# Kernel tuning notes

Hardware: AMD Instinct MI355X
Metric: run time of the kernel (lower is better)

## Reference

```python
import jax, jax.numpy as jnp
import numpy as np

D, H, W = 128, 96, 96  # voxel grid
EPS = 1e-5

_OFFS = np.array([[dz, dy, dx] for dz in (-1, 0, 1) for dy in (-1, 0, 1) for dx in (-1, 0, 1)], dtype=np.int64)


def _flat(c):
    return (c[:, 0] * H + c[:, 1]) * W + c[:, 2]


def _dilate(coords):
    # union of coords + all 27 offsets, clipped to grid bounds (stride-1, pad-1 SparseConv3d output sites)
    p = coords[None, :, :] + _OFFS[:, None, :]          # [27, N, 3]
    p = p.reshape(-1, 3)
    ok = np.all((p >= 0) & (p < np.array([D, H, W])), axis=1)
    keys = np.unique(_flat(p[ok]))
    out = np.stack([keys // (H * W), (keys // W) % H, keys % W], axis=1)
    return out


def _rulebook(in_coords, out_coords):
    # nb[k, m] = row index into in_coords of (out_coords[m] + off_k), or -1
    lut = -np.ones(D * H * W, dtype=np.int32)
    lut[_flat(in_coords)] = np.arange(len(in_coords), dtype=np.int32)
    nb = np.full((27, len(out_coords)), -1, dtype=np.int32)
    for k, o in enumerate(_OFFS):
        p = out_coords + o
        ok = np.all((p >= 0) & (p < np.array([D, H, W])), axis=1)
        nb[k, ok] = lut[_flat(p[ok])]
    return nb


def setup_inputs() -> dict:
    key = jax.random.key(0)
    ks = jax.random.split(key, 20)
    # active sites: full plane z=64 over 96x96 footprint (surface-like sparse scene)
    yy, xx = np.meshgrid(np.arange(H), np.arange(W), indexing='ij')
    coords0 = np.stack([np.full(H * W, 64), yy.ravel(), xx.ravel()], axis=1).astype(np.int64)
    coords1 = _dilate(coords0)   # 27648 sites
    coords2 = _dilate(coords1)   # 46080 sites
    nb1 = jnp.asarray(_rulebook(coords0, coords1))
    nbs = jnp.asarray(_rulebook(coords1, coords1))
    nb2 = jnp.asarray(_rulebook(coords1, coords2))

    s = 0.05
    inp = {
        'x': jax.random.normal(ks[0], (coords0.shape[0], 256), jnp.float32),
        'w_s1': jax.random.normal(ks[1], (27, 256, 128), jnp.float32) * s,
        'g_s1': jax.random.uniform(ks[2], (128,), jnp.float32, 0.5, 1.5),
        'b_s1': jax.random.normal(ks[3], (128,), jnp.float32) * 0.1,
        'w11': jax.random.normal(ks[4], (27, 128, 128), jnp.float32) * s,
        'g11': jax.random.uniform(ks[5], (128,), jnp.float32, 0.5, 1.5),
        'b11': jax.random.normal(ks[6], (128,), jnp.float32) * 0.1,
        'w12': jax.random.normal(ks[7], (27, 128, 128), jnp.float32) * s,
        'g12': jax.random.uniform(ks[8], (128,), jnp.float32, 0.5, 1.5),
        'b12': jax.random.normal(ks[9], (128,), jnp.float32) * 0.1,
        'w21': jax.random.normal(ks[10], (27, 128, 128), jnp.float32) * s,
        'g21': jax.random.uniform(ks[11], (128,), jnp.float32, 0.5, 1.5),
        'b21': jax.random.normal(ks[12], (128,), jnp.float32) * 0.1,
        'w22': jax.random.normal(ks[13], (27, 128, 128), jnp.float32) * s,
        'g22': jax.random.uniform(ks[14], (128,), jnp.float32, 0.5, 1.5),
        'b22': jax.random.normal(ks[15], (128,), jnp.float32) * 0.1,
        'w_s2': jax.random.normal(ks[16], (27, 128, 32), jnp.float32) * s,
        'g_s2': jax.random.uniform(ks[17], (32,), jnp.float32, 0.5, 1.5),
        'b_s2': jax.random.normal(ks[18], (32,), jnp.float32) * 0.1,
        'nb1': nb1, 'nbs': nbs, 'nb2': nb2,
    }
    return inp


def _sparse_conv(x, nb, w):
    # gather -> GEMM -> accumulate per kernel offset (rulebook semantics of spconv)
    mask = nb >= 0                      # [27, M]
    idx = jnp.where(mask, nb, 0)
    out = jnp.zeros((nb.shape[1], w.shape[2]), x.dtype)
    for k in range(nb.shape[0]):        # fixed 27-offset loop
        g = jnp.where(mask[k][:, None], x[idx[k]], 0.0)  # [M, Cin]
        out = out + g @ w[k]
    return out


def _bn(f, g, b):
    # BatchNorm1d in training mode over active voxel rows (biased variance)
    mu = jnp.mean(f, axis=0)
    var = jnp.mean(jnp.square(f - mu), axis=0)
    return (f - mu) * jax.lax.rsqrt(var + EPS) * g + b


def _block(f, nbs, w1, g1, b1, w2, g2, b2):
    idn = f
    h = jax.nn.relu(_bn(_sparse_conv(f, nbs, w1), g1, b1))
    h = _bn(_sparse_conv(h, nbs, w2), g2, b2)
    return jax.nn.relu(h + idn)


def reference(x, w_s1, g_s1, b_s1, w11, g11, b11, w12, g12, b12,
              w21, g21, b21, w22, g22, b22, w_s2, g_s2, b_s2,
              nb1, nbs, nb2):
    f = jax.nn.relu(_bn(_sparse_conv(x, nb1, w_s1), g_s1, b_s1))          # spconv1
    f = _block(f, nbs, w11, g11, b11, w12, g12, b12)                      # block1 (submanifold)
    f = _block(f, nbs, w21, g21, b21, w22, g22, b22)                      # block2 (submanifold)
    out = jax.nn.relu(_bn(_sparse_conv(f, nb2, w_s2), g_s2, b_s2))        # spconv2
    return out  # features of the final SparseConvTensor, [46080, 32]
```

## Files before the change

### kernel.cpp

```cpp
#include <hip/hip_runtime.h>
#include <stdint.h>

typedef _Float16 f16;
typedef _Float16 f16x8 __attribute__((ext_vector_type(8)));
typedef _Float16 f16x4 __attribute__((ext_vector_type(4)));
typedef float f32x4 __attribute__((ext_vector_type(4)));

#define GAS __attribute__((address_space(1)))
#define LAS __attribute__((address_space(3)))

__device__ __forceinline__ void gl_lds16(const void* g, void* l) {
    __builtin_amdgcn_global_load_lds((const GAS uint32_t*)g, (LAS uint32_t*)l, 16, 0, 0);
}

__global__ __launch_bounds__(256) void prep(
    const float* __restrict__ x, f16* __restrict__ xh, long nx4,
    const float* __restrict__ ws1, f16* __restrict__ w1,
    const float* __restrict__ w11, f16* __restrict__ wa1,
    const float* __restrict__ w12, f16* __restrict__ wa2,
    const float* __restrict__ w21, f16* __restrict__ wb1,
    const float* __restrict__ w22, f16* __restrict__ wb2,
    const float* __restrict__ ws2, f16* __restrict__ w2,
    float* __restrict__ zbuf, long nz, int nbzc) {
    if ((int)blockIdx.x < nbzc) {
        long t = (long)blockIdx.x * 256 + threadIdx.x;
        if (t < nz) { zbuf[t] = 0.f; return; }
        t -= nz;
        if (t < nx4) {
            float4 v = ((const float4*)x)[t];
            f16x4 o = {(f16)v.x, (f16)v.y, (f16)v.z, (f16)v.w};
            *(f16x4*)(xh + t * 4) = o;
        }
        return;
    }
    int tau = blockIdx.x - nbzc;
    const float* src; f16* dst; int Cin, Cout;
    if (tau < 864)        { src = ws1; dst = w1;  Cin = 256; Cout = 128; }
    else if (tau < 1296)  { tau -= 864;  src = w11; dst = wa1; Cin = 128; Cout = 128; }
    else if (tau < 1728)  { tau -= 1296; src = w12; dst = wa2; Cin = 128; Cout = 128; }
    else if (tau < 2160)  { tau -= 1728; src = w21; dst = wb1; Cin = 128; Cout = 128; }
    else if (tau < 2592)  { tau -= 2160; src = w22; dst = wb2; Cin = 128; Cout = 128; }
    else                  { tau -= 2592; src = ws2; dst = w2;  Cin = 128; Cout = 32; }
    const int nci = Cin >> 5, nco = Cout >> 5;
    const int k  = tau / (nci * nco);
    const int rm = tau - k * nci * nco;
    const int ci0 = (rm / nco) << 5;
    const int co0 = (rm % nco) << 5;
    __shared__ float tile[32][33];
    const int r = threadIdx.x >> 5, c = threadIdx.x & 31;
#pragma unroll
    for (int i2 = 0; i2 < 4; i2++)
        tile[r + 8 * i2][c] =
            src[((long)(k * Cin + ci0 + r + 8 * i2)) * Cout + co0 + c];
    __syncthreads();
#pragma unroll
    for (int i2 = 0; i2 < 4; i2++)
        dst[((long)(k * Cout + co0 + r + 8 * i2)) * Cin + ci0 + c] =
            (f16)tile[c][r + 8 * i2];
}

template <int LAYER>
__global__ __launch_bounds__(512, 2) void conv_dense(
    const f16* __restrict__ fin, const f16* __restrict__ wt,
    const f16* __restrict__ zrow, float* __restrict__ out,
    float* __restrict__ stats) {
    constexpr int COUT = (LAYER == 2) ? 32 : 128;
    constexpr int INRB = (LAYER == 0) ? 512 : 256;
    constexpr int WRB  = (LAYER == 0) ? 512 : 256;
    constexpr int RT   = (COUT == 128) ? 4 : 2;
    constexpr int CT   = (COUT == 128) ? 4 : 2;
    constexpr int NBCH = COUT / 4;
    extern __shared__ char smem[];
    char* ldsA0 = smem;
    char* ldsA1 = smem + 46080;
    char* ldsB0 = smem + 92160;
    char* ldsB1 = smem + 92160 + COUT * 256;

    const int b = blockIdx.x;
    const int p = b / 72;
    const int t0 = b % 72;
    const int y0 = (t0 / 6) * 8;
    const int x0 = (t0 % 6) * 16;
    const int tid = threadIdx.x;
    const int lane = tid & 63;
    const int wave = tid >> 6;
    const int kh = wave & 1;
    const int pairId = wave >> 1;
    const int q = lane >> 4;
    const int r16 = lane & 15;
    const int wr = ((COUT == 128) ? (pairId >> 1) : pairId) * (RT * 16);
    const int wc = ((COUT == 128) ? (pairId & 1) : 0) * (CT * 16);

    int S = 0;
    int js[3], dzs[3], hs[3];
    if (LAYER == 0) {
        js[0] = 0; dzs[0] = 1 - p; hs[0] = 0;
        js[1] = 0; dzs[1] = 1 - p; hs[1] = 1;
        S = 2;
    } else {
        for (int dz = -1; dz <= 1; dz++) {
            int j = (LAYER == 1) ? p + dz : p + dz - 1;
            if (0 <= j && j < 3) { js[S] = j; dzs[S] = dz; hs[S] = 0; S++; }
        }
    }

    auto stageA = [&](int s, char* buf) {
        const int j = js[s], h = hs[s];
        const long pbase = (long)j * 9216;
        for (int ch = wave; ch < 45; ch += 8) {
            int site = ch * 4 + q;
            int sy = site / 18;
            int sx = site - sy * 18;
            int y = y0 - 1 + sy;
            int x = x0 - 1 + sx;
            int cc = r16 ^ (site & 7);
            bool ok = ((unsigned)y < 96u) & ((unsigned)x < 96u);
            const char* src = ok
                ? (const char*)fin + (pbase + y * 96 + x) * INRB + h * 256 + cc * 16
                : (const char*)zrow + cc * 16;
            gl_lds16(src, buf + ch * 1024);
        }
    };
    auto stageB = [&](int k, int h, char* buf) {
        for (int ch = wave; ch < NBCH; ch += 8) {
            int col = ch * 4 + q;
            int cc = r16 ^ (col & 7);
            const char* src = (const char*)wt + (long)(k * COUT + col) * WRB +
                              h * 256 + cc * 16;
            gl_lds16(src, buf + ch * 1024);
        }
    };

    f32x4 acc[RT][CT];
#pragma unroll
    for (int tr = 0; tr < RT; tr++)
#pragma unroll
        for (int c = 0; c < CT; c++) acc[tr][c] = f32x4{0.f, 0.f, 0.f, 0.f};

    stageA(0, ldsA0);
    stageB((dzs[0] + 1) * 9, hs[0], ldsB0);

    int tap = 0;
    for (int s = 0; s < S; s++) {
        const char* bufA = (s & 1) ? ldsA1 : ldsA0;
#pragma unroll
        for (int i = 0; i < 9; i++, tap++) {
            __syncthreads();
            if (i == 0 && s + 1 < S) stageA(s + 1, ((s + 1) & 1) ? ldsA1 : ldsA0);
            if (tap + 1 < S * 9) {
                int sn = (i == 8) ? s + 1 : s;
                int in2 = (i == 8) ? 0 : i + 1;
                stageB((dzs[sn] + 1) * 9 + in2, hs[sn], ((tap + 1) & 1) ? ldsB1 : ldsB0);
            }
            const char* bufB = (tap & 1) ? ldsB1 : ldsB0;
            const int dy = i / 3 - 1, dx = i % 3 - 1;
#pragma unroll
            for (int kk2 = 0; kk2 < 2; kk2++) {
                const int kk = kh * 2 + kk2;
                f16x8 Af[RT], Bf[CT];
#pragma unroll
                for (int tr = 0; tr < RT; tr++) {
                    int site = (wr / 16 + tr + 1 + dy) * 18 + 1 + dx + r16;
                    Af[tr] = *(const f16x8*)(bufA + site * 256 +
                                             (((kk * 4 + q) ^ (site & 7)) << 4));
                }
#pragma unroll
                for (int c = 0; c < CT; c++) {
                    int col = wc + c * 16 + r16;
                    Bf[c] = *(const f16x8*)(bufB + col * 256 +
                                            (((kk * 4 + q) ^ (col & 7)) << 4));
                }
#pragma unroll
                for (int tr = 0; tr < RT; tr++)
#pragma unroll
                    for (int c = 0; c < CT; c++)
                        acc[tr][c] = __builtin_amdgcn_mfma_f32_16x16x32_f16(
                            Af[tr], Bf[c], acc[tr][c], 0, 0, 0);
            }
        }
    }

    char* xch = smem + 92160;
    constexpr int XR = RT * CT * 1024;
    __syncthreads();
    if (kh == 1) {
#pragma unroll
        for (int tr = 0; tr < RT; tr++)
#pragma unroll
            for (int c = 0; c < CT; c++)
                *(f32x4*)(xch + pairId * XR + (tr * CT + c) * 1024 + lane * 16) =
                    acc[tr][c];
    }
    __syncthreads();
    if (kh == 1) return;
#pragma unroll
    for (int tr = 0; tr < RT; tr++)
#pragma unroll
        for (int c = 0; c < CT; c++)
            acc[tr][c] += *(const f32x4*)(xch + pairId * XR + (tr * CT + c) * 1024 +
                                          lane * 16);

    const long mbase = (long)p * 9216 + (long)y0 * 96 + x0;
#pragma unroll
    for (int c = 0; c < CT; c++) {
        const int col = wc + c * 16 + r16;
        float sum = 0.f, ssq = 0.f;
#pragma unroll
        for (int tr = 0; tr < RT; tr++) {
            const int ly = wr / 16 + tr;
#pragma unroll
            for (int r = 0; r < 4; r++) {
                const int lx = q * 4 + r;
                float v = acc[tr][c][r];
                out[(mbase + ly * 96 + lx) * COUT + col] = v;
                sum += v;
                ssq = fmaf(v, v, ssq);
            }
        }
        sum += __shfl_xor(sum, 16);
        sum += __shfl_xor(sum, 32);
        ssq += __shfl_xor(ssq, 16);
        ssq += __shfl_xor(ssq, 32);
        if (q == 0) {
            atomicAdd(&stats[col], sum);
            atomicAdd(&stats[COUT + col], ssq);
        }
    }
}

__global__ __launch_bounds__(256) void bn_apply4(
    const float4* __restrict__ f, const float* __restrict__ sums,
    const float* __restrict__ g, const float* __restrict__ bta,
    const f16x4* __restrict__ idn, f16* __restrict__ outh,
    float4* __restrict__ outf, long n4, int C, float invM) {
    long i = (long)blockIdx.x * 256 + threadIdx.x;
    if (i >= n4) return;
    int col0 = (int)((i * 4) & (C - 1));
    float4 v = f[i];
    float r[4] = {v.x, v.y, v.z, v.w};
    f16x4 id = {};
    if (idn) id = idn[i];
    f16x4 ho;
#pragma unroll
    for (int j = 0; j < 4; j++) {
        int c = col0 + j;
        float mu = sums[c] * invM;
        float var = sums[C + c] * invM - mu * mu;
        var = fmaxf(var, 0.f);
        float sc = g[c] * rsqrtf(var + 1e-5f);
        float x = (r[j] - mu) * sc + bta[c];
        if (idn) x += (float)id[j];
        x = fmaxf(x, 0.f);
        r[j] = x;
        ho[j] = (f16)x;
    }
    if (outf) outf[i] = make_float4(r[0], r[1], r[2], r[3]);
    else *(f16x4*)(outh + i * 4) = ho;
}

extern "C" void kernel_launch(void* const* d_in, const int* in_sizes, int n_in,
                              void* d_out, int out_size, void* d_ws, size_t ws_size,
                              hipStream_t stream) {
    (void)n_in; (void)out_size; (void)ws_size;
    const float* x    = (const float*)d_in[0];
    const float* w_s1 = (const float*)d_in[1];
    const float* g_s1 = (const float*)d_in[2];
    const float* b_s1 = (const float*)d_in[3];
    const float* w11  = (const float*)d_in[4];
    const float* g11  = (const float*)d_in[5];
    const float* b11  = (const float*)d_in[6];
    const float* w12  = (const float*)d_in[7];
    const float* g12  = (const float*)d_in[8];
    const float* b12  = (const float*)d_in[9];
    const float* w21  = (const float*)d_in[10];
    const float* g21  = (const float*)d_in[11];
    const float* b21  = (const float*)d_in[12];
    const float* w22  = (const float*)d_in[13];
    const float* g22  = (const float*)d_in[14];
    const float* b22  = (const float*)d_in[15];
    const float* w_s2 = (const float*)d_in[16];
    const float* g_s2 = (const float*)d_in[17];
    const float* b_s2 = (const float*)d_in[18];

    const int N0 = in_sizes[0] / 256;
    const int M1 = in_sizes[19] / 27;
    const int M2 = in_sizes[21] / 27;

    char* base = (char*)d_ws;
    size_t off = 0;
    auto alloc = [&](size_t bytes) -> char* {
        off = (off + 255) & ~(size_t)255;
        char* p = base + off;
        off += bytes;
        return p;
    };
    f16* xh  = (f16*)alloc((size_t)N0 * 256 * 2);
    f16* w1  = (f16*)alloc(27UL * 128 * 256 * 2);
    f16* wa1 = (f16*)alloc(27UL * 128 * 128 * 2);
    f16* wa2 = (f16*)alloc(27UL * 128 * 128 * 2);
    f16* wb1 = (f16*)alloc(27UL * 128 * 128 * 2);
    f16* wb2 = (f16*)alloc(27UL * 128 * 128 * 2);
    f16* w2  = (f16*)alloc(27UL * 32 * 128 * 2);
    f16* fA  = (f16*)alloc((size_t)M1 * 128 * 2);
    f16* fB  = (f16*)alloc((size_t)M1 * 128 * 2);
    float* cbuf  = (float*)alloc((size_t)M1 * 128 * 4);
    float* stats = (float*)alloc(1344UL * 4);
    f16*   zrow  = (f16*)alloc(512);

    const int lds01 = 92160 + 2 * 128 * 256;
    const int lds2  = 92160 + 2 * 32 * 256;
    (void)hipFuncSetAttribute((const void*)conv_dense<0>,
                              hipFuncAttributeMaxDynamicSharedMemorySize, lds01);
    (void)hipFuncSetAttribute((const void*)conv_dense<1>,
                              hipFuncAttributeMaxDynamicSharedMemorySize, lds01);
    (void)hipFuncSetAttribute((const void*)conv_dense<2>,
                              hipFuncAttributeMaxDynamicSharedMemorySize, lds2);

    const long nz  = 1472;
    const long nx4 = (long)N0 * 256 / 4;
    const int nbzc = (int)((nz + nx4 + 255) / 256);
    prep<<<nbzc + 2700, 256, 0, stream>>>(
        x, xh, nx4, w_s1, w1, w11, wa1, w12, wa2, w21, wb1, w22, wb2,
        w_s2, w2, stats, nz, nbzc);

    const float inv1 = 1.f / (float)M1, inv2 = 1.f / (float)M2;
    const int g1 = 3 * 72;
    const int g2 = 5 * 72;
    const long n4a = (long)M1 * 128 / 4;
    const long n4b = (long)M2 * 32 / 4;
    const int ga = (int)((n4a + 255) / 256);
    const int gb = (int)((n4b + 255) / 256);

    conv_dense<0><<<g1, 512, lds01, stream>>>(xh, w1, zrow, cbuf, stats);
    bn_apply4<<<ga, 256, 0, stream>>>((float4*)cbuf, stats, g_s1, b_s1,
                                      nullptr, fA, nullptr, n4a, 128, inv1);
    conv_dense<1><<<g1, 512, lds01, stream>>>(fA, wa1, zrow, cbuf, stats + 256);
    bn_apply4<<<ga, 256, 0, stream>>>((float4*)cbuf, stats + 256, g11, b11,
                                      nullptr, fB, nullptr, n4a, 128, inv1);
    conv_dense<1><<<g1, 512, lds01, stream>>>(fB, wa2, zrow, cbuf, stats + 512);
    bn_apply4<<<ga, 256, 0, stream>>>((float4*)cbuf, stats + 512, g12, b12,
                                      (const f16x4*)fA, fA, nullptr, n4a, 128, inv1);
    conv_dense<1><<<g1, 512, lds01, stream>>>(fA, wb1, zrow, cbuf, stats + 768);
    bn_apply4<<<ga, 256, 0, stream>>>((float4*)cbuf, stats + 768, g21, b21,
                                      nullptr, fB, nullptr, n4a, 128, inv1);
    conv_dense<1><<<g1, 512, lds01, stream>>>(fB, wb2, zrow, cbuf, stats + 1024);
    bn_apply4<<<ga, 256, 0, stream>>>((float4*)cbuf, stats + 1024, g22, b22,
                                      (const f16x4*)fA, fA, nullptr, n4a, 128, inv1);
    conv_dense<2><<<g2, 512, lds2, stream>>>(fA, w2, zrow, cbuf, stats + 1280);
    bn_apply4<<<gb, 256, 0, stream>>>((float4*)cbuf, stats + 1280, g_s2, b_s2,
                                      nullptr, nullptr, (float4*)d_out, n4b, 32, inv2);
}
```

Measured before the change: 378.1 us.

## Fold BatchNorm+ReLU of previous layer into conv input staging, store raw outputs fp16

Conv outputs are now stored as fp16 instead of fp32, halving the raw-output write and read traffic. For the second conv of each block and for the final spconv, the previous layer's BN scale/shift, ReLU and optional residual add are applied while staging input tiles into LDS. This removes three bn_apply passes. The cost is that these layers use register loads plus LDS stores instead of async global-to-LDS copies, and every halo site is normalised again by each tile that reads it. Storing raw pre-BN values in fp16 also adds some rounding error.

```diff
diff --git a/kernel.cpp b/kernel.cpp
--- a/kernel.cpp
+++ b/kernel.cpp
@@ -59,11 +59,14 @@
             (f16)tile[c][r + 8 * i2];
 }
 
-template <int LAYER>
+template <int LAYER, bool FOLD, bool RESID>
 __global__ __launch_bounds__(512, 2) void conv_dense(
     const f16* __restrict__ fin, const f16* __restrict__ wt,
-    const f16* __restrict__ zrow, float* __restrict__ out,
-    float* __restrict__ stats) {
+    const f16* __restrict__ zrow, f16* __restrict__ out,
+    float* __restrict__ stats,
+    const float* __restrict__ pstats, const float* __restrict__ pg,
+    const float* __restrict__ pb, const f16* __restrict__ resid,
+    float pinv) {
     constexpr int COUT = (LAYER == 2) ? 32 : 128;
     constexpr int INRB = (LAYER == 0) ? 512 : 256;
     constexpr int WRB  = (LAYER == 0) ? 512 : 256;
@@ -104,6 +107,19 @@
         }
     }
 
+    float psc[8], pbt[8];
+    if (FOLD) {
+#pragma unroll
+        for (int e = 0; e < 8; e++) {
+            int c = r16 * 8 + e;
+            float mu = pstats[c] * pinv;
+            float var = fmaxf(pstats[128 + c] * pinv - mu * mu, 0.f);
+            float s = pg[c] * rsqrtf(var + 1e-5f);
+            psc[e] = s;
+            pbt[e] = pb[c] - mu * s;
+        }
+    }
+
     auto stageA = [&](int s, char* buf) {
         const int j = js[s], h = hs[s];
         const long pbase = (long)j * 9216;
@@ -113,12 +129,29 @@
             int sx = site - sy * 18;
             int y = y0 - 1 + sy;
             int x = x0 - 1 + sx;
-            int cc = r16 ^ (site & 7);
             bool ok = ((unsigned)y < 96u) & ((unsigned)x < 96u);
-            const char* src = ok
-                ? (const char*)fin + (pbase + y * 96 + x) * INRB + h * 256 + cc * 16
-                : (const char*)zrow + cc * 16;
-            gl_lds16(src, buf + ch * 1024);
+            if (FOLD) {
+                f16x8 o = {};
+                if (ok) {
+                    const long ro = (pbase + y * 96 + x) * 128 + r16 * 8;
+                    f16x8 v = *(const f16x8*)(fin + ro);
+                    f16x8 rv = {};
+                    if (RESID) rv = *(const f16x8*)(resid + ro);
+#pragma unroll
+                    for (int e = 0; e < 8; e++) {
+                        float t = (float)v[e] * psc[e] + pbt[e];
+                        if (RESID) t += (float)rv[e];
+                        o[e] = (f16)fmaxf(t, 0.f);
+                    }
+                }
+                *(f16x8*)(buf + site * 256 + ((r16 ^ (site & 7)) << 4)) = o;
+            } else {
+                int cc = r16 ^ (site & 7);
+                const char* src = ok
+                    ? (const char*)fin + (pbase + y * 96 + x) * INRB + h * 256 + cc * 16
+                    : (const char*)zrow + cc * 16;
+                gl_lds16(src, buf + ch * 1024);
+            }
         }
     };
     auto stageB = [&](int k, int h, char* buf) {
@@ -212,7 +245,7 @@
             for (int r = 0; r < 4; r++) {
                 const int lx = q * 4 + r;
                 float v = acc[tr][c][r];
-                out[(mbase + ly * 96 + lx) * COUT + col] = v;
+                out[(mbase + ly * 96 + lx) * COUT + col] = (f16)v;
                 sum += v;
                 ssq = fmaf(v, v, ssq);
             }
@@ -228,34 +261,38 @@
     }
 }
 
-__global__ __launch_bounds__(256) void bn_apply4(
-    const float4* __restrict__ f, const float* __restrict__ sums,
+__global__ __launch_bounds__(256) void bn_apply8(
+    const f16x8* __restrict__ f, const float* __restrict__ sums,
     const float* __restrict__ g, const float* __restrict__ bta,
-    const f16x4* __restrict__ idn, f16* __restrict__ outh,
-    float4* __restrict__ outf, long n4, int C, float invM) {
+    const f16x8* __restrict__ idn, f16* __restrict__ outh,
+    float* __restrict__ outf, long n8, int C, float invM) {
     long i = (long)blockIdx.x * 256 + threadIdx.x;
-    if (i >= n4) return;
-    int col0 = (int)((i * 4) & (C - 1));
-    float4 v = f[i];
-    float r[4] = {v.x, v.y, v.z, v.w};
-    f16x4 id = {};
+    if (i >= n8) return;
+    int col0 = (int)((i * 8) & (C - 1));
+    f16x8 v = f[i];
+    f16x8 id = {};
     if (idn) id = idn[i];
-    f16x4 ho;
-#pragma unroll
-    for (int j = 0; j < 4; j++) {
+    f16x8 ho;
+    float ro[8];
+#pragma unroll
+    for (int j = 0; j < 8; j++) {
         int c = col0 + j;
         float mu = sums[c] * invM;
         float var = sums[C + c] * invM - mu * mu;
         var = fmaxf(var, 0.f);
         float sc = g[c] * rsqrtf(var + 1e-5f);
-        float x = (r[j] - mu) * sc + bta[c];
+        float x = ((float)v[j] - mu) * sc + bta[c];
         if (idn) x += (float)id[j];
         x = fmaxf(x, 0.f);
-        r[j] = x;
+        ro[j] = x;
         ho[j] = (f16)x;
     }
-    if (outf) outf[i] = make_float4(r[0], r[1], r[2], r[3]);
-    else *(f16x4*)(outh + i * 4) = ho;
+    if (outf) {
+        *(float4*)(outf + i * 8)     = make_float4(ro[0], ro[1], ro[2], ro[3]);
+        *(float4*)(outf + i * 8 + 4) = make_float4(ro[4], ro[5], ro[6], ro[7]);
+    } else {
+        *(f16x8*)(outh + i * 8) = ho;
+    }
 }
 
 extern "C" void kernel_launch(void* const* d_in, const int* in_sizes, int n_in,
@@ -302,18 +339,22 @@
     f16* wb2 = (f16*)alloc(27UL * 128 * 128 * 2);
     f16* w2  = (f16*)alloc(27UL * 32 * 128 * 2);
     f16* fA  = (f16*)alloc((size_t)M1 * 128 * 2);
-    f16* fB  = (f16*)alloc((size_t)M1 * 128 * 2);
-    float* cbuf  = (float*)alloc((size_t)M1 * 128 * 4);
+    f16* fC  = (f16*)alloc((size_t)M1 * 128 * 2);
+    f16* rA  = (f16*)alloc((size_t)M1 * 128 * 2);
+    f16* rB  = (f16*)alloc((size_t)M1 * 128 * 2);
+    f16* rS2 = (f16*)alloc((size_t)M2 * 32 * 2);
     float* stats = (float*)alloc(1344UL * 4);
     f16*   zrow  = (f16*)alloc(512);
 
     const int lds01 = 92160 + 2 * 128 * 256;
     const int lds2  = 92160 + 2 * 32 * 256;
-    (void)hipFuncSetAttribute((const void*)conv_dense<0>,
+    (void)hipFuncSetAttribute((const void*)conv_dense<0, false, false>,
                               hipFuncAttributeMaxDynamicSharedMemorySize, lds01);
-    (void)hipFuncSetAttribute((const void*)conv_dense<1>,
+    (void)hipFuncSetAttribute((const void*)conv_dense<1, false, false>,
                               hipFuncAttributeMaxDynamicSharedMemorySize, lds01);
-    (void)hipFuncSetAttribute((const void*)conv_dense<2>,
+    (void)hipFuncSetAttribute((const void*)conv_dense<1, true, false>,
+                              hipFuncAttributeMaxDynamicSharedMemorySize, lds01);
+    (void)hipFuncSetAttribute((const void*)conv_dense<2, true, true>,
                               hipFuncAttributeMaxDynamicSharedMemorySize, lds2);
 
     const long nz  = 1472;
@@ -326,27 +367,27 @@
     const float inv1 = 1.f / (float)M1, inv2 = 1.f / (float)M2;
     const int g1 = 3 * 72;
     const int g2 = 5 * 72;
-    const long n4a = (long)M1 * 128 / 4;
-    const long n4b = (long)M2 * 32 / 4;
-    const int ga = (int)((n4a + 255) / 256);
-    const int gb = (int)((n4b + 255) / 256);
-
-    conv_dense<0><<<g1, 512, lds01, stream>>>(xh, w1, zrow, cbuf, stats);
-    bn_apply4<<<ga, 256, 0, stream>>>((float4*)cbuf, stats, g_s1, b_s1,
-                                      nullptr, fA, nullptr, n4a, 128, inv1);
-    conv_dense<1><<<g1, 512, lds01, stream>>>(fA, wa1, zrow, cbuf, stats + 256);
-    bn_apply4<<<ga, 256, 0, stream>>>((float4*)cbuf, stats + 256, g11, b11,
-                                      nullptr, fB, nullptr, n4a, 128, inv1);
-    conv_dense<1><<<g1, 512, lds01, stream>>>(fB, wa2, zrow, cbuf, stats + 512);
-    bn_apply4<<<ga, 256, 0, stream>>>((float4*)cbuf, stats + 512, g12, b12,
-                                      (const f16x4*)fA, fA, nullptr, n4a, 128, inv1);
-    conv_dense<1><<<g1, 512, lds01, stream>>>(fA, wb1, zrow, cbuf, stats + 768);
-    bn_apply4<<<ga, 256, 0, stream>>>((float4*)cbuf, stats + 768, g21, b21,
-                                      nullptr, fB, nullptr, n4a, 128, inv1);
-    conv_dense<1><<<g1, 512, lds01, stream>>>(fB, wb2, zrow, cbuf, stats + 1024);
-    bn_apply4<<<ga, 256, 0, stream>>>((float4*)cbuf, stats + 1024, g22, b22,
-                                      (const f16x4*)fA, fA, nullptr, n4a, 128, inv1);
-    conv_dense<2><<<g2, 512, lds2, stream>>>(fA, w2, zrow, cbuf, stats + 1280);
-    bn_apply4<<<gb, 256, 0, stream>>>((float4*)cbuf, stats + 1280, g_s2, b_s2,
-                                      nullptr, nullptr, (float4*)d_out, n4b, 32, inv2);
-}
+    const long n8a = (long)M1 * 128 / 8;
+    const long n8b = (long)M2 * 32 / 8;
+    const int ga = (int)((n8a + 255) / 256);
+    const int gb = (int)((n8b + 255) / 256);
+
+    conv_dense<0, false, false><<<g1, 512, lds01, stream>>>(
+        xh, w1, zrow, rA, stats, nullptr, nullptr, nullptr, nullptr, 0.f);
+    bn_apply8<<<ga, 256, 0, stream>>>((const f16x8*)rA, stats, g_s1, b_s1,
+                                      nullptr, fA, nullptr, n8a, 128, inv1);
+    conv_dense<1, false, false><<<g1, 512, lds01, stream>>>(
+        fA, wa1, zrow, rB, stats + 256, nullptr, nullptr, nullptr, nullptr, 0.f);
+    conv_dense<1, true, false><<<g1, 512, lds01, stream>>>(
+        rB, wa2, zrow, rA, stats + 512, stats + 256, g11, b11, nullptr, inv1);
+    bn_apply8<<<ga, 256, 0, stream>>>((const f16x8*)rA, stats + 512, g12, b12,
+                                      (const f16x8*)fA, fC, nullptr, n8a, 128, inv1);
+    conv_dense<1, false, false><<<g1, 512, lds01, stream>>>(
+        fC, wb1, zrow, rB, stats + 768, nullptr, nullptr, nullptr, nullptr, 0.f);
+    conv_dense<1, true, false><<<g1, 512, lds01, stream>>>(
+        rB, wb2, zrow, rA, stats + 1024, stats + 768, g21, b21, nullptr, inv1);
+    conv_dense<2, true, true><<<g2, 512, lds2, stream>>>(
+        rA, w2, zrow, rS2, stats + 1280, stats + 1024, g22, b22, fC, inv1);
+    bn_apply8<<<gb, 256, 0, stream>>>((const f16x8*)rS2, stats + 1280, g_s2, b_s2,
+                                      nullptr, nullptr, (float*)d_out, n8b, 32, inv2);
+}
```

Result: faster. 356.5 us (-5.7%).
